# Kernel optimization log

Hardware: AMD Instinct MI355X
Metric: run time of the kernel (lower is better)

The kernel has to match this reference:

```python
import jax, jax.numpy as jnp
import numpy as np

B, T = 32, 4096
I_CND2 = 512      # 2 * size_i_cnd
EMB = 256         # size_i_embed_ar
H = 896           # size_h_rnn
FC = 896          # size_h_fc
O = 512           # size_o


def setup_inputs() -> dict:
    key = jax.random.key(0)
    ks = jax.random.split(key, 8)
    s = 0.02
    return {
        "reference_sample": jax.random.randint(ks[0], (B, T), 0, O),
        "i_cnd_series": jax.random.normal(ks[1], (B, T, I_CND2), dtype=jnp.float32),
        "emb": jax.random.normal(ks[2], (O, EMB), dtype=jnp.float32) * s,
        "w_ih": jax.random.normal(ks[3], (3 * H, EMB + I_CND2), dtype=jnp.float32) * s,
        "w_hh": jax.random.normal(ks[4], (3 * H, H), dtype=jnp.float32) * s,
        "b_ih": jnp.zeros((3 * H,), jnp.float32),
        "b_hh": jnp.zeros((3 * H,), jnp.float32),
        "fc1_w": jax.random.normal(ks[5], (FC, H), dtype=jnp.float32) * s,
        "fc1_b": jnp.zeros((FC,), jnp.float32),
        "fc2_w": jax.random.normal(ks[6], (O, FC), dtype=jnp.float32) * s,
        "fc2_b": jnp.zeros((O,), jnp.float32),
    }


def _gru_scan(gates_x, w_hh, b_hh):
    # gates_x: (B, T, 3H) precomputed input projections (torch gate order: r, z, n)
    h0 = jnp.zeros((gates_x.shape[0], H), gates_x.dtype)

    def step(h, gx):
        gh = h @ w_hh.T + b_hh
        xr, xz, xn = jnp.split(gx, 3, axis=-1)
        hr, hz, hn = jnp.split(gh, 3, axis=-1)
        r = jax.nn.sigmoid(xr + hr)
        z = jax.nn.sigmoid(xz + hz)
        n = jnp.tanh(xn + r * hn)
        h_new = (1.0 - z) * n + z * h
        return h_new, h_new

    _, hs = jax.lax.scan(step, h0, jnp.swapaxes(gates_x, 0, 1))  # (T, B, H)
    return jnp.swapaxes(hs, 0, 1)  # (B, T, H)


def reference(reference_sample, i_cnd_series, emb, w_ih, w_hh, b_ih, b_hh,
              fc1_w, fc1_b, fc2_w, fc2_b):
    # embedding + concat with conditioning
    x = jnp.concatenate([emb[reference_sample], i_cnd_series], axis=-1)  # (B,T,EMB+2C)
    # batch all input-side GRU matmuls (compute-dense), scan only hidden recurrence
    gates_x = jnp.einsum('btd,gd->btg', x, w_ih) + b_ih  # (B,T,3H)
    o_rnn = _gru_scan(gates_x, w_hh, b_hh)               # (B,T,H)
    hidden = jax.nn.relu(jnp.einsum('bth,fh->btf', o_rnn, fc1_w) + fc1_b)
    return jnp.einsum('btf,of->bto', hidden, fc2_w) + fc2_b  # (B,T,O)
```

## Files before the change

### kernel.cpp

```cpp
#include <hip/hip_runtime.h>

#define B_ 32
#define T_FULL 4096
#define EMB_ 256
#define XD_ 768
#define H_ 896
#define G3_ 2688
#define O_ 512
#define NWG_SCAN 28
#define UJ 32
#define THR_SCAN 768

typedef __attribute__((ext_vector_type(8))) short bf16x8;
typedef __attribute__((ext_vector_type(4))) float f32x4;

__device__ __forceinline__ f32x4 mfma16(bf16x8 a, bf16x8 b, f32x4 c) {
  return __builtin_amdgcn_mfma_f32_16x16x32_bf16(a, b, c, 0, 0, 0);
}

__device__ __forceinline__ unsigned short f2bf(float x) {
  union { float f; unsigned u; } v; v.f = x;
  unsigned r = v.u + 0x7fffu + ((v.u >> 16) & 1u);
  return (unsigned short)(r >> 16);
}
__device__ __forceinline__ float bf2f(unsigned short h) {
  union { float f; unsigned u; } v; v.u = ((unsigned)h) << 16;
  return v.f;
}

__device__ __forceinline__ unsigned long long aload64(const unsigned long long* p) {
  return __hip_atomic_load((unsigned long long*)p, __ATOMIC_RELAXED, __HIP_MEMORY_SCOPE_AGENT);
}
__device__ __forceinline__ unsigned aload32(const unsigned* p) {
  return __hip_atomic_load((unsigned*)p, __ATOMIC_RELAXED, __HIP_MEMORY_SCOPE_AGENT);
}
__device__ __forceinline__ void astore32(unsigned* p, unsigned v) {
  __hip_atomic_store(p, v, __ATOMIC_RELAXED, __HIP_MEMORY_SCOPE_AGENT);
}

__global__ __launch_bounds__(256) void cvt_bf16(const float* __restrict__ in,
                                                unsigned short* __restrict__ out, int n) {
  for (int i = blockIdx.x * 256 + threadIdx.x; i < n; i += gridDim.x * 256)
    out[i] = f2bf(in[i]);
}

template<int VAR>
__global__ __launch_bounds__(256) void gemm_bf16(
    const unsigned short* __restrict__ A,
    const int* __restrict__ sample,
    const float* __restrict__ icnd,
    const unsigned short* __restrict__ embb,
    const unsigned short* __restrict__ W,
    const float* __restrict__ bias,
    float* __restrict__ outf,
    unsigned short* __restrict__ outb,
    int t0) {
  constexpr int K = (VAR == 0) ? XD_ : H_;
  constexpr int N = (VAR == 0) ? G3_ : (VAR == 1 ? H_ : O_);
  constexpr int LDT = 48;
  __shared__ __align__(16) unsigned short Asl[128 * LDT];
  __shared__ __align__(16) unsigned short Bsl[128 * LDT];
  const int tid = threadIdx.x;
  const int rowBase = blockIdx.y * 128, colBase = blockIdx.x * 128;
  const int lane = tid & 63, wid = tid >> 6;
  const int wm = wid >> 1, wn = wid & 1;
  const int lr = lane & 15, lk = lane >> 4;
  const f32x4 fzero = {0.f, 0.f, 0.f, 0.f};
  f32x4 acc[4][4];
#pragma unroll
  for (int i = 0; i < 4; ++i)
#pragma unroll
    for (int j = 0; j < 4; ++j) acc[i][j] = fzero;

  for (int k0 = 0; k0 < K; k0 += 32) {
#pragma unroll
    for (int s = 0; s < 2; ++s) {
      const int seg = tid + s * 256;
      const int r = seg >> 2, kg = (seg & 3) * 8;
      const int kk = k0 + kg;
      bf16x8 va;
      if (VAR == 0) {
        const int rowG = rowBase + r;
        const int b = rowG & 31, t = t0 + (rowG >> 5);
        if (kk < EMB_) {
          const int e = sample[b * T_FULL + t];
          va = *(const bf16x8*)(embb + e * EMB_ + kk);
        } else {
          const float* p = icnd + ((size_t)(b * T_FULL + t)) * 512 + (kk - EMB_);
          const float4 f0 = *(const float4*)p;
          const float4 f1 = *(const float4*)(p + 4);
          va[0] = (short)f2bf(f0.x); va[1] = (short)f2bf(f0.y);
          va[2] = (short)f2bf(f0.z); va[3] = (short)f2bf(f0.w);
          va[4] = (short)f2bf(f1.x); va[5] = (short)f2bf(f1.y);
          va[6] = (short)f2bf(f1.z); va[7] = (short)f2bf(f1.w);
        }
      } else {
        va = *(const bf16x8*)(A + (size_t)(rowBase + r) * K + kk);
      }
      *(bf16x8*)(Asl + r * LDT + kg) = va;
      *(bf16x8*)(Bsl + r * LDT + kg) = *(const bf16x8*)(W + (size_t)(colBase + r) * K + kk);
    }
    __syncthreads();
    bf16x8 af[4], bfr[4];
#pragma unroll
    for (int mt = 0; mt < 4; ++mt)
      af[mt] = *(const bf16x8*)(Asl + (wm * 64 + mt * 16 + lr) * LDT + lk * 8);
#pragma unroll
    for (int nt = 0; nt < 4; ++nt)
      bfr[nt] = *(const bf16x8*)(Bsl + (wn * 64 + nt * 16 + lr) * LDT + lk * 8);
#pragma unroll
    for (int mt = 0; mt < 4; ++mt)
#pragma unroll
      for (int nt = 0; nt < 4; ++nt) acc[mt][nt] = mfma16(af[mt], bfr[nt], acc[mt][nt]);
    __syncthreads();
  }

#pragma unroll
  for (int mt = 0; mt < 4; ++mt) {
#pragma unroll
    for (int nt = 0; nt < 4; ++nt) {
      const int colG = colBase + wn * 64 + nt * 16 + lr;
      const float bv = bias[colG];
#pragma unroll
      for (int r = 0; r < 4; ++r) {
        const int rowG = rowBase + wm * 64 + mt * 16 + lk * 4 + r;
        const float v = acc[mt][nt][r] + bv;
        if (VAR == 0) {
          outf[(size_t)rowG * N + colG] = v;
        } else if (VAR == 1) {
          outb[(size_t)rowG * N + colG] = f2bf(fmaxf(v, 0.f));
        } else {
          const int b = rowG & 31, t = t0 + (rowG >> 5);
          outf[((size_t)(b * T_FULL + t)) * O_ + colG] = v;
        }
      }
    }
  }
}

__global__ __launch_bounds__(THR_SCAN) void scan_gru(
    const float* __restrict__ gates,
    const unsigned short* __restrict__ whh,
    const float* __restrict__ bhh,
    unsigned short* __restrict__ hhi,
    unsigned short* __restrict__ hlo,
    unsigned short* __restrict__ ornn,
    unsigned int* __restrict__ arr,
    int t0, int Tc) {
  __shared__ __align__(16) unsigned short hst[2][32 * H_];
  __shared__ float gh[3][32][UJ + 1];
  const int tid = threadIdx.x;
  const int j0 = blockIdx.x * UJ;
  const int lane = tid & 63, wid = tid >> 6;
  const int m = wid & 1;
  const int s = (wid >> 1) % 3;
  const int cn = wid / 6;
  const int lr = lane & 15, lk = lane >> 4;
  char* hbase = (char*)&hst[0][0];

  const int eb = tid >> 4, ec = (tid & 15) * 2;
  float hown0 = 0.f, hown1 = 0.f;
  float bh_r0 = 0.f, bh_r1 = 0.f, bh_z0 = 0.f, bh_z1 = 0.f, bh_n0 = 0.f, bh_n1 = 0.f;
  if (tid < 512) {
    const int j = j0 + ec;
    bh_r0 = bhh[j];          bh_r1 = bhh[j + 1];
    bh_z0 = bhh[H_ + j];     bh_z1 = bhh[H_ + j + 1];
    bh_n0 = bhh[2 * H_ + j]; bh_n1 = bhh[2 * H_ + j + 1];
    const int rb0 = (t0 + 1) & 1;
    const int o = rb0 * (32 * H_) + eb * H_ + j;
    const unsigned hi01 = aload32((const unsigned*)(hhi + o));
    const unsigned lo01 = aload32((const unsigned*)(hlo + o));
    hown0 = bf2f((unsigned short)(hi01 & 0xffff)) + bf2f((unsigned short)(lo01 & 0xffff));
    hown1 = bf2f((unsigned short)(hi01 >> 16)) + bf2f((unsigned short)(lo01 >> 16));
  }

  const unsigned short* wp = whh + (size_t)(s * H_ + j0 + cn * 16 + lr) * H_ + lk * 8;
  const int rrow = m * 16 + lr;
  const int rowb = rrow * 1792;
  const int sw_r = (rrow & 7) << 4;
  const f32x4 fzero = {0.f, 0.f, 0.f, 0.f};

  for (int tl = 0; tl < Tc; ++tl) {
    const int t = t0 + tl;
    const int rb = (t + 1) & 1, wb = t & 1;

    float2 pxr = {0.f, 0.f}, pxz = {0.f, 0.f}, pxn = {0.f, 0.f};
    if (tid < 512) {
      const float* gx = gates + ((size_t)tl * 32 + eb) * G3_;
      pxr = *(const float2*)(gx + j0 + ec);
      pxz = *(const float2*)(gx + H_ + j0 + ec);
      pxn = *(const float2*)(gx + 2 * H_ + j0 + ec);
    }

    {
      const unsigned long long* sh = (const unsigned long long*)(hhi + rb * (32 * H_));
      const unsigned long long* sl = (const unsigned long long*)(hlo + rb * (32 * H_));
#pragma unroll
      for (int k = 0; k < 10; ++k) {
        const int i = tid + k * THR_SCAN;
        if (i < 7168) {
          const unsigned long long vh = aload64(sh + i);
          const unsigned long long vl = aload64(sl + i);
          const int row = i / 224;
          const int cb = (i - row * 224) * 8;
          const int dst = row * 1792 + (cb ^ ((row & 7) << 4));
          *(unsigned long long*)(hbase + dst) = vh;
          *(unsigned long long*)(hbase + 57344 + dst) = vl;
        }
      }
    }
    __syncthreads();

    f32x4 a0 = fzero, a1 = fzero;
#pragma unroll
    for (int kk = 0; kk < 28; ++kk) {
      const int off = (lk * 16 + kk * 64) ^ sw_r;
      const bf16x8 ah = *(const bf16x8*)(hbase + rowb + off);
      const bf16x8 al = *(const bf16x8*)(hbase + 57344 + rowb + off);
      const bf16x8 bw = *(const bf16x8*)(wp + kk * 32);
      a0 = mfma16(ah, bw, a0);
      a1 = mfma16(al, bw, a1);
    }
#pragma unroll
    for (int r = 0; r < 4; ++r) gh[s][m * 16 + lk * 4 + r][cn * 16 + lr] = a0[r] + a1[r];
    __syncthreads();

    if (tid < 512) {
      const float ghr0 = gh[0][eb][ec] + bh_r0, ghr1 = gh[0][eb][ec + 1] + bh_r1;
      const float ghz0 = gh[1][eb][ec] + bh_z0, ghz1 = gh[1][eb][ec + 1] + bh_z1;
      const float ghn0 = gh[2][eb][ec] + bh_n0, ghn1 = gh[2][eb][ec + 1] + bh_n1;
      const float r0 = 1.f / (1.f + __expf(-(pxr.x + ghr0)));
      const float r1 = 1.f / (1.f + __expf(-(pxr.y + ghr1)));
      const float z0 = 1.f / (1.f + __expf(-(pxz.x + ghz0)));
      const float z1 = 1.f / (1.f + __expf(-(pxz.y + ghz1)));
      const float e0 = __expf(2.f * (pxn.x + r0 * ghn0));
      const float e1 = __expf(2.f * (pxn.y + r1 * ghn1));
      const float n0 = 1.f - 2.f / (e0 + 1.f);
      const float n1 = 1.f - 2.f / (e1 + 1.f);
      hown0 = (1.f - z0) * n0 + z0 * hown0;
      hown1 = (1.f - z1) * n1 + z1 * hown1;
      const unsigned short h0 = f2bf(hown0), h1 = f2bf(hown1);
      const unsigned short l0 = f2bf(hown0 - bf2f(h0)), l1 = f2bf(hown1 - bf2f(h1));
      const unsigned hi01 = (unsigned)h0 | ((unsigned)h1 << 16);
      const unsigned lo01 = (unsigned)l0 | ((unsigned)l1 << 16);
      const int o = wb * (32 * H_) + eb * H_ + j0 + ec;
      astore32((unsigned*)(hhi + o), hi01);
      astore32((unsigned*)(hlo + o), lo01);
      *(unsigned*)(ornn + ((size_t)tl * 32 + eb) * H_ + j0 + ec) = hi01;
    }

    asm volatile("s_waitcnt vmcnt(0)" ::: "memory");
    __syncthreads();
    if (wid == 0) {
      const unsigned tgt = (unsigned)(t + 1);
      if (lane == 0) astore32(arr + blockIdx.x, tgt);
      for (;;) {
        const unsigned v = (lane < NWG_SCAN) ? aload32(arr + lane) : tgt;
        if (__all(v >= tgt)) break;
        __builtin_amdgcn_s_sleep(1);
      }
    }
    __syncthreads();
  }
}

extern "C" void kernel_launch(void* const* d_in, const int* in_sizes, int n_in,
                              void* d_out, int out_size, void* d_ws, size_t ws_size,
                              hipStream_t stream) {
  (void)in_sizes; (void)n_in; (void)out_size;
  const int* sample = (const int*)d_in[0];
  const float* icnd = (const float*)d_in[1];
  const float* emb = (const float*)d_in[2];
  const float* wih = (const float*)d_in[3];
  const float* whh = (const float*)d_in[4];
  const float* bih = (const float*)d_in[5];
  const float* bhh = (const float*)d_in[6];
  const float* fc1w = (const float*)d_in[7];
  const float* fc1b = (const float*)d_in[8];
  const float* fc2w = (const float*)d_in[9];
  const float* fc2b = (const float*)d_in[10];
  float* out = (float*)d_out;
  char* ws = (char*)d_ws;

  size_t off = 0;
  auto alloc = [&](size_t bytes) {
    size_t o = off;
    off = (off + bytes + 255) & ~(size_t)255;
    return o;
  };
  const size_t o_arr = alloc(256);
  const size_t o_hhi = alloc((size_t)2 * 32 * H_ * 2);
  const size_t o_hlo = alloc((size_t)2 * 32 * H_ * 2);
  const size_t zero_end = off;
  const size_t o_emb = alloc((size_t)O_ * EMB_ * 2);
  const size_t o_wih = alloc((size_t)G3_ * XD_ * 2);
  const size_t o_whh = alloc((size_t)G3_ * H_ * 2);
  const size_t o_f1w = alloc((size_t)H_ * H_ * 2);
  const size_t o_f2w = alloc((size_t)O_ * H_ * 2);
  const size_t head = off;

  int Tc = 512;
  while (Tc > 8) {
    size_t need = head + (size_t)Tc * 32 * G3_ * 4 + 2 * ((size_t)Tc * 32 * H_ * 2) + 4096;
    if (need <= ws_size) break;
    Tc >>= 1;
  }
  const size_t o_gat = alloc((size_t)Tc * 32 * G3_ * 4);
  const size_t o_orn = alloc((size_t)Tc * 32 * H_ * 2);
  const size_t o_hid = alloc((size_t)Tc * 32 * H_ * 2);
  (void)o_gat; (void)o_orn; (void)o_hid;

  unsigned short* embb = (unsigned short*)(ws + o_emb);
  unsigned short* wihb = (unsigned short*)(ws + o_wih);
  unsigned short* whhb = (unsigned short*)(ws + o_whh);
  unsigned short* f1wb = (unsigned short*)(ws + o_f1w);
  unsigned short* f2wb = (unsigned short*)(ws + o_f2w);
  float* gat = (float*)(ws + o_gat);
  unsigned short* orn = (unsigned short*)(ws + o_orn);
  unsigned short* hid = (unsigned short*)(ws + o_hid);
  unsigned short* hhi = (unsigned short*)(ws + o_hhi);
  unsigned short* hlo = (unsigned short*)(ws + o_hlo);
  unsigned int* arr = (unsigned int*)(ws + o_arr);

  (void)hipMemsetAsync(ws, 0, zero_end, stream);

  cvt_bf16<<<512, 256, 0, stream>>>(emb, embb, O_ * EMB_);
  cvt_bf16<<<1024, 256, 0, stream>>>(wih, wihb, G3_ * XD_);
  cvt_bf16<<<1024, 256, 0, stream>>>(whh, whhb, G3_ * H_);
  cvt_bf16<<<512, 256, 0, stream>>>(fc1w, f1wb, H_ * H_);
  cvt_bf16<<<512, 256, 0, stream>>>(fc2w, f2wb, O_ * H_);

  const int nch = T_FULL / Tc;
  const int M = Tc * 32;
  for (int c = 0; c < nch; ++c) {
    const int t0 = c * Tc;
    gemm_bf16<0><<<dim3(G3_ / 128, M / 128), 256, 0, stream>>>(
        nullptr, sample, icnd, embb, wihb, bih, gat, nullptr, t0);
    scan_gru<<<NWG_SCAN, THR_SCAN, 0, stream>>>(gat, whhb, bhh, hhi, hlo, orn, arr, t0, Tc);
    gemm_bf16<1><<<dim3(H_ / 128, M / 128), 256, 0, stream>>>(
        orn, nullptr, nullptr, nullptr, f1wb, fc1b, nullptr, hid, t0);
    gemm_bf16<2><<<dim3(O_ / 128, M / 128), 256, 0, stream>>>(
        hid, nullptr, nullptr, nullptr, f2wb, fc2b, out, nullptr, t0);
  }
}
```

Before: 39.14 ms.

## Restructure GRU scan to 512 threads with fused hidden buffer and prefetch

```diff
diff --git a/kernel.cpp b/kernel.cpp
--- a/kernel.cpp
+++ b/kernel.cpp
@@ -8,8 +8,7 @@
 #define G3_ 2688
 #define O_ 512
 #define NWG_SCAN 28
-#define UJ 32
-#define THR_SCAN 768
+#define THR_SCAN 512
 
 typedef __attribute__((ext_vector_type(8))) short bf16x8;
 typedef __attribute__((ext_vector_type(4))) float f32x4;
@@ -142,93 +141,111 @@
     const float* __restrict__ gates,
     const unsigned short* __restrict__ whh,
     const float* __restrict__ bhh,
-    unsigned short* __restrict__ hhi,
-    unsigned short* __restrict__ hlo,
+    unsigned long long* __restrict__ hbuf,
     unsigned short* __restrict__ ornn,
     unsigned int* __restrict__ arr,
     int t0, int Tc) {
-  __shared__ __align__(16) unsigned short hst[2][32 * H_];
-  __shared__ float gh[3][32][UJ + 1];
+  __shared__ __align__(16) char hst[114688];
+  __shared__ float gh2[96][33];
   const int tid = threadIdx.x;
-  const int j0 = blockIdx.x * UJ;
+  const int j0 = blockIdx.x * 32;
   const int lane = tid & 63, wid = tid >> 6;
-  const int m = wid & 1;
-  const int s = (wid >> 1) % 3;
-  const int cn = wid / 6;
   const int lr = lane & 15, lk = lane >> 4;
-  char* hbase = (char*)&hst[0][0];
-
+  const int m = wid & 1, cw = wid >> 1;
   const int eb = tid >> 4, ec = (tid & 15) * 2;
-  float hown0 = 0.f, hown1 = 0.f;
-  float bh_r0 = 0.f, bh_r1 = 0.f, bh_z0 = 0.f, bh_z1 = 0.f, bh_n0 = 0.f, bh_n1 = 0.f;
-  if (tid < 512) {
+
+  float bh0, bh1, bh2, bh3, bh4, bh5;
+  float hown0, hown1;
+  {
     const int j = j0 + ec;
-    bh_r0 = bhh[j];          bh_r1 = bhh[j + 1];
-    bh_z0 = bhh[H_ + j];     bh_z1 = bhh[H_ + j + 1];
-    bh_n0 = bhh[2 * H_ + j]; bh_n1 = bhh[2 * H_ + j + 1];
+    bh0 = bhh[j];          bh1 = bhh[j + 1];
+    bh2 = bhh[H_ + j];     bh3 = bhh[H_ + j + 1];
+    bh4 = bhh[2 * H_ + j]; bh5 = bhh[2 * H_ + j + 1];
     const int rb0 = (t0 + 1) & 1;
-    const int o = rb0 * (32 * H_) + eb * H_ + j;
-    const unsigned hi01 = aload32((const unsigned*)(hhi + o));
-    const unsigned lo01 = aload32((const unsigned*)(hlo + o));
+    const unsigned short* hb = (const unsigned short*)hbuf;
+    const unsigned hi01 = aload32((const unsigned*)(hb + rb0 * 57344 + eb * 896 + j));
+    const unsigned lo01 = aload32((const unsigned*)(hb + rb0 * 57344 + 28672 + eb * 896 + j));
     hown0 = bf2f((unsigned short)(hi01 & 0xffff)) + bf2f((unsigned short)(lo01 & 0xffff));
     hown1 = bf2f((unsigned short)(hi01 >> 16)) + bf2f((unsigned short)(lo01 >> 16));
   }
 
-  const unsigned short* wp = whh + (size_t)(s * H_ + j0 + cn * 16 + lr) * H_ + lk * 8;
-  const int rrow = m * 16 + lr;
-  const int rowb = rrow * 1792;
-  const int sw_r = (rrow & 7) << 4;
+  const unsigned short* wp0;
+  const unsigned short* wp1;
+  const unsigned short* wp2;
+  {
+    const int cwc = (cw < 2) ? cw : 0;
+    const int t0i = cwc * 3;
+    wp0 = whh + (size_t)((t0i >> 1) * H_ + j0 + ((t0i & 1) << 4) + lr) * H_ + lk * 8;
+    const int t1i = cwc * 3 + 1;
+    wp1 = whh + (size_t)((t1i >> 1) * H_ + j0 + ((t1i & 1) << 4) + lr) * H_ + lk * 8;
+    const int t2i = cwc * 3 + 2;
+    wp2 = whh + (size_t)((t2i >> 1) * H_ + j0 + ((t2i & 1) << 4) + lr) * H_ + lk * 8;
+  }
+  const int rowb = (m * 16 + lr) * 1792;
+  const int sw = (lr & 7) << 4;
   const f32x4 fzero = {0.f, 0.f, 0.f, 0.f};
+
+  float2 pxr, pxz, pxn;
+  {
+    const float* gx = gates + (size_t)eb * G3_;
+    pxr = *(const float2*)(gx + j0 + ec);
+    pxz = *(const float2*)(gx + H_ + j0 + ec);
+    pxn = *(const float2*)(gx + 2 * H_ + j0 + ec);
+  }
 
   for (int tl = 0; tl < Tc; ++tl) {
     const int t = t0 + tl;
     const int rb = (t + 1) & 1, wb = t & 1;
 
-    float2 pxr = {0.f, 0.f}, pxz = {0.f, 0.f}, pxn = {0.f, 0.f};
-    if (tid < 512) {
-      const float* gx = gates + ((size_t)tl * 32 + eb) * G3_;
-      pxr = *(const float2*)(gx + j0 + ec);
-      pxz = *(const float2*)(gx + H_ + j0 + ec);
-      pxn = *(const float2*)(gx + 2 * H_ + j0 + ec);
-    }
-
     {
-      const unsigned long long* sh = (const unsigned long long*)(hhi + rb * (32 * H_));
-      const unsigned long long* sl = (const unsigned long long*)(hlo + rb * (32 * H_));
-#pragma unroll
-      for (int k = 0; k < 10; ++k) {
-        const int i = tid + k * THR_SCAN;
-        if (i < 7168) {
-          const unsigned long long vh = aload64(sh + i);
-          const unsigned long long vl = aload64(sl + i);
-          const int row = i / 224;
-          const int cb = (i - row * 224) * 8;
-          const int dst = row * 1792 + (cb ^ ((row & 7) << 4));
-          *(unsigned long long*)(hbase + dst) = vh;
-          *(unsigned long long*)(hbase + 57344 + dst) = vl;
-        }
-      }
-    }
-    __syncthreads();
-
-    f32x4 a0 = fzero, a1 = fzero;
-#pragma unroll
-    for (int kk = 0; kk < 28; ++kk) {
-      const int off = (lk * 16 + kk * 64) ^ sw_r;
-      const bf16x8 ah = *(const bf16x8*)(hbase + rowb + off);
-      const bf16x8 al = *(const bf16x8*)(hbase + 57344 + rowb + off);
-      const bf16x8 bw = *(const bf16x8*)(wp + kk * 32);
-      a0 = mfma16(ah, bw, a0);
-      a1 = mfma16(al, bw, a1);
-    }
-#pragma unroll
-    for (int r = 0; r < 4; ++r) gh[s][m * 16 + lk * 4 + r][cn * 16 + lr] = a0[r] + a1[r];
-    __syncthreads();
-
-    if (tid < 512) {
-      const float ghr0 = gh[0][eb][ec] + bh_r0, ghr1 = gh[0][eb][ec + 1] + bh_r1;
-      const float ghz0 = gh[1][eb][ec] + bh_z0, ghz1 = gh[1][eb][ec + 1] + bh_z1;
-      const float ghn0 = gh[2][eb][ec] + bh_n0, ghn1 = gh[2][eb][ec + 1] + bh_n1;
+      const unsigned long long* src = hbuf + (size_t)rb * 14336 + tid;
+      unsigned long long rg[28];
+#pragma unroll
+      for (int k = 0; k < 28; ++k) rg[k] = aload64(src + k * 512);
+#pragma unroll
+      for (int k = 0; k < 28; ++k) {
+        const int i = tid + k * 512;
+        const int p = (i >= 7168) ? 1 : 0;
+        const int w = i - p * 7168;
+        const int row = (int)(((unsigned)w * 18725u) >> 22);
+        const int cb = (w - row * 224) * 8;
+        const int dst = p * 57344 + row * 1792 + (cb ^ ((row & 7) << 4));
+        *(unsigned long long*)(hst + dst) = rg[k];
+      }
+    }
+    __syncthreads();
+
+    if (wid < 4) {
+      f32x4 acc[3][2];
+#pragma unroll
+      for (int u = 0; u < 3; ++u) { acc[u][0] = fzero; acc[u][1] = fzero; }
+#pragma unroll
+      for (int kk = 0; kk < 28; ++kk) {
+        const int off = (lk * 16 + kk * 64) ^ sw;
+        const bf16x8 ah = *(const bf16x8*)(hst + rowb + off);
+        const bf16x8 al = *(const bf16x8*)(hst + 57344 + rowb + off);
+        const bf16x8 b0 = *(const bf16x8*)(wp0 + kk * 32);
+        acc[0][0] = mfma16(ah, b0, acc[0][0]);
+        acc[0][1] = mfma16(al, b0, acc[0][1]);
+        const bf16x8 b1 = *(const bf16x8*)(wp1 + kk * 32);
+        acc[1][0] = mfma16(ah, b1, acc[1][0]);
+        acc[1][1] = mfma16(al, b1, acc[1][1]);
+        const bf16x8 b2 = *(const bf16x8*)(wp2 + kk * 32);
+        acc[2][0] = mfma16(ah, b2, acc[2][0]);
+        acc[2][1] = mfma16(al, b2, acc[2][1]);
+      }
+#pragma unroll
+      for (int u = 0; u < 3; ++u)
+#pragma unroll
+        for (int r = 0; r < 4; ++r)
+          gh2[(cw * 3 + u) * 16 + lr][m * 16 + lk * 4 + r] = acc[u][0][r] + acc[u][1][r];
+    }
+    __syncthreads();
+
+    {
+      const float ghr0 = gh2[ec][eb] + bh0,      ghr1 = gh2[ec + 1][eb] + bh1;
+      const float ghz0 = gh2[32 + ec][eb] + bh2, ghz1 = gh2[33 + ec][eb] + bh3;
+      const float ghn0 = gh2[64 + ec][eb] + bh4, ghn1 = gh2[65 + ec][eb] + bh5;
       const float r0 = 1.f / (1.f + __expf(-(pxr.x + ghr0)));
       const float r1 = 1.f / (1.f + __expf(-(pxr.y + ghr1)));
       const float z0 = 1.f / (1.f + __expf(-(pxz.x + ghz0)));
@@ -243,17 +260,24 @@
       const unsigned short l0 = f2bf(hown0 - bf2f(h0)), l1 = f2bf(hown1 - bf2f(h1));
       const unsigned hi01 = (unsigned)h0 | ((unsigned)h1 << 16);
       const unsigned lo01 = (unsigned)l0 | ((unsigned)l1 << 16);
-      const int o = wb * (32 * H_) + eb * H_ + j0 + ec;
-      astore32((unsigned*)(hhi + o), hi01);
-      astore32((unsigned*)(hlo + o), lo01);
-      *(unsigned*)(ornn + ((size_t)tl * 32 + eb) * H_ + j0 + ec) = hi01;
+      unsigned short* hb = (unsigned short*)hbuf;
+      const int o = wb * 57344 + eb * 896 + j0 + ec;
+      astore32((unsigned*)(hb + o), hi01);
+      astore32((unsigned*)(hb + o + 28672), lo01);
+      *(unsigned*)(ornn + ((size_t)tl * 32 + eb) * 896 + j0 + ec) = hi01;
     }
 
     asm volatile("s_waitcnt vmcnt(0)" ::: "memory");
     __syncthreads();
+    const unsigned tgt = (unsigned)(t + 1);
+    if (tid == 0) astore32(arr + blockIdx.x, tgt);
+    if (tl + 1 < Tc) {
+      const float* gx = gates + ((size_t)(tl + 1) * 32 + eb) * G3_;
+      pxr = *(const float2*)(gx + j0 + ec);
+      pxz = *(const float2*)(gx + H_ + j0 + ec);
+      pxn = *(const float2*)(gx + 2 * H_ + j0 + ec);
+    }
     if (wid == 0) {
-      const unsigned tgt = (unsigned)(t + 1);
-      if (lane == 0) astore32(arr + blockIdx.x, tgt);
       for (;;) {
         const unsigned v = (lane < NWG_SCAN) ? aload32(arr + lane) : tgt;
         if (__all(v >= tgt)) break;
@@ -289,8 +313,7 @@
     return o;
   };
   const size_t o_arr = alloc(256);
-  const size_t o_hhi = alloc((size_t)2 * 32 * H_ * 2);
-  const size_t o_hlo = alloc((size_t)2 * 32 * H_ * 2);
+  const size_t o_h = alloc((size_t)2 * 2 * 32 * H_ * 2);
   const size_t zero_end = off;
   const size_t o_emb = alloc((size_t)O_ * EMB_ * 2);
   const size_t o_wih = alloc((size_t)G3_ * XD_ * 2);
@@ -318,8 +341,7 @@
   float* gat = (float*)(ws + o_gat);
   unsigned short* orn = (unsigned short*)(ws + o_orn);
   unsigned short* hid = (unsigned short*)(ws + o_hid);
-  unsigned short* hhi = (unsigned short*)(ws + o_hhi);
-  unsigned short* hlo = (unsigned short*)(ws + o_hlo);
+  unsigned long long* hbuf = (unsigned long long*)(ws + o_h);
   unsigned int* arr = (unsigned int*)(ws + o_arr);
 
   (void)hipMemsetAsync(ws, 0, zero_end, stream);
@@ -336,7 +358,7 @@
     const int t0 = c * Tc;
     gemm_bf16<0><<<dim3(G3_ / 128, M / 128), 256, 0, stream>>>(
         nullptr, sample, icnd, embb, wihb, bih, gat, nullptr, t0);
-    scan_gru<<<NWG_SCAN, THR_SCAN, 0, stream>>>(gat, whhb, bhh, hhi, hlo, orn, arr, t0, Tc);
+    scan_gru<<<NWG_SCAN, THR_SCAN, 0, stream>>>(gat, whhb, bhh, hbuf, orn, arr, t0, Tc);
     gemm_bf16<1><<<dim3(H_ / 128, M / 128), 256, 0, stream>>>(
         orn, nullptr, nullptr, nullptr, f1wb, fc1b, nullptr, hid, t0);
     gemm_bf16<2><<<dim3(O_ / 128, M / 128), 256, 0, stream>>>(
```

New measurement: 55.31 ms. 41.3% more time.

## Keep W_hh in registers, use 32x32 MFMA, pre-swizzled global hidden state

Applied to the files above, without the earlier changes.

```diff
diff --git a/kernel.cpp b/kernel.cpp
--- a/kernel.cpp
+++ b/kernel.cpp
@@ -8,14 +8,17 @@
 #define G3_ 2688
 #define O_ 512
 #define NWG_SCAN 28
-#define UJ 32
 #define THR_SCAN 768
 
 typedef __attribute__((ext_vector_type(8))) short bf16x8;
 typedef __attribute__((ext_vector_type(4))) float f32x4;
+typedef __attribute__((ext_vector_type(16))) float f32x16;
 
 __device__ __forceinline__ f32x4 mfma16(bf16x8 a, bf16x8 b, f32x4 c) {
   return __builtin_amdgcn_mfma_f32_16x16x32_bf16(a, b, c, 0, 0, 0);
+}
+__device__ __forceinline__ f32x16 mfma32(bf16x8 a, bf16x8 b, f32x16 c) {
+  return __builtin_amdgcn_mfma_f32_32x32x16_bf16(a, b, c, 0, 0, 0);
 }
 
 __device__ __forceinline__ unsigned short f2bf(float x) {
@@ -36,6 +39,12 @@
 }
 __device__ __forceinline__ void astore32(unsigned* p, unsigned v) {
   __hip_atomic_store(p, v, __ATOMIC_RELAXED, __HIP_MEMORY_SCOPE_AGENT);
+}
+
+__device__ __forceinline__ int hswz(int row, int cb) {
+  const int g = cb >> 4;
+  const int gs = (g & ~15) | ((g & 15) ^ (row & 15));
+  return row * 1792 + (gs << 4) + (cb & 15);
 }
 
 __global__ __launch_bounds__(256) void cvt_bf16(const float* __restrict__ in,
@@ -142,48 +151,52 @@
     const float* __restrict__ gates,
     const unsigned short* __restrict__ whh,
     const float* __restrict__ bhh,
-    unsigned short* __restrict__ hhi,
-    unsigned short* __restrict__ hlo,
+    unsigned long long* __restrict__ hbuf,
     unsigned short* __restrict__ ornn,
     unsigned int* __restrict__ arr,
     int t0, int Tc) {
-  __shared__ __align__(16) unsigned short hst[2][32 * H_];
-  __shared__ float gh[3][32][UJ + 1];
+  __shared__ __align__(16) char hst[114688];
+  __shared__ float gh2f[2 * 96 * 32];
   const int tid = threadIdx.x;
-  const int j0 = blockIdx.x * UJ;
+  const int j0 = blockIdx.x * 32;
   const int lane = tid & 63, wid = tid >> 6;
-  const int m = wid & 1;
-  const int s = (wid >> 1) % 3;
-  const int cn = wid / 6;
-  const int lr = lane & 15, lk = lane >> 4;
-  char* hbase = (char*)&hst[0][0];
-
+  const int l31 = lane & 31, lhi = lane >> 5;
+  const int s = wid >> 2, kq = wid & 3;
+  const int ph = kq >> 1;
   const int eb = tid >> 4, ec = (tid & 15) * 2;
+
+  bf16x8 wreg[14];
+  {
+    const unsigned short* wrow = whh + (size_t)(s * H_ + j0 + l31) * H_ + kq * 224 + lhi * 8;
+#pragma unroll
+    for (int i = 0; i < 14; ++i) wreg[i] = *(const bf16x8*)(wrow + i * 16);
+  }
+
+  float bh0 = 0.f, bh1 = 0.f, bh2 = 0.f, bh3 = 0.f, bh4 = 0.f, bh5 = 0.f;
   float hown0 = 0.f, hown1 = 0.f;
-  float bh_r0 = 0.f, bh_r1 = 0.f, bh_z0 = 0.f, bh_z1 = 0.f, bh_n0 = 0.f, bh_n1 = 0.f;
   if (tid < 512) {
     const int j = j0 + ec;
-    bh_r0 = bhh[j];          bh_r1 = bhh[j + 1];
-    bh_z0 = bhh[H_ + j];     bh_z1 = bhh[H_ + j + 1];
-    bh_n0 = bhh[2 * H_ + j]; bh_n1 = bhh[2 * H_ + j + 1];
+    bh0 = bhh[j];          bh1 = bhh[j + 1];
+    bh2 = bhh[H_ + j];     bh3 = bhh[H_ + j + 1];
+    bh4 = bhh[2 * H_ + j]; bh5 = bhh[2 * H_ + j + 1];
     const int rb0 = (t0 + 1) & 1;
-    const int o = rb0 * (32 * H_) + eb * H_ + j;
-    const unsigned hi01 = aload32((const unsigned*)(hhi + o));
-    const unsigned lo01 = aload32((const unsigned*)(hlo + o));
+    const char* hb = (const char*)hbuf + rb0 * 114688;
+    const int off = hswz(eb, 2 * j);
+    const unsigned hi01 = aload32((const unsigned*)(hb + off));
+    const unsigned lo01 = aload32((const unsigned*)(hb + off + 57344));
     hown0 = bf2f((unsigned short)(hi01 & 0xffff)) + bf2f((unsigned short)(lo01 & 0xffff));
     hown1 = bf2f((unsigned short)(hi01 >> 16)) + bf2f((unsigned short)(lo01 >> 16));
   }
-
-  const unsigned short* wp = whh + (size_t)(s * H_ + j0 + cn * 16 + lr) * H_ + lk * 8;
-  const int rrow = m * 16 + lr;
-  const int rowb = rrow * 1792;
-  const int sw_r = (rrow & 7) << 4;
-  const f32x4 fzero = {0.f, 0.f, 0.f, 0.f};
 
   for (int tl = 0; tl < Tc; ++tl) {
     const int t = t0 + tl;
     const int rb = (t + 1) & 1, wb = t & 1;
 
+    {
+      const f32x4 z4 = {0.f, 0.f, 0.f, 0.f};
+      *(f32x4*)(gh2f + tid * 8) = z4;
+      *(f32x4*)(gh2f + tid * 8 + 4) = z4;
+    }
     float2 pxr = {0.f, 0.f}, pxz = {0.f, 0.f}, pxn = {0.f, 0.f};
     if (tid < 512) {
       const float* gx = gates + ((size_t)tl * 32 + eb) * G3_;
@@ -191,44 +204,61 @@
       pxz = *(const float2*)(gx + H_ + j0 + ec);
       pxn = *(const float2*)(gx + 2 * H_ + j0 + ec);
     }
-
     {
-      const unsigned long long* sh = (const unsigned long long*)(hhi + rb * (32 * H_));
-      const unsigned long long* sl = (const unsigned long long*)(hlo + rb * (32 * H_));
-#pragma unroll
-      for (int k = 0; k < 10; ++k) {
-        const int i = tid + k * THR_SCAN;
-        if (i < 7168) {
-          const unsigned long long vh = aload64(sh + i);
-          const unsigned long long vl = aload64(sl + i);
-          const int row = i / 224;
-          const int cb = (i - row * 224) * 8;
-          const int dst = row * 1792 + (cb ^ ((row & 7) << 4));
-          *(unsigned long long*)(hbase + dst) = vh;
-          *(unsigned long long*)(hbase + 57344 + dst) = vl;
-        }
-      }
-    }
-    __syncthreads();
-
-    f32x4 a0 = fzero, a1 = fzero;
-#pragma unroll
-    for (int kk = 0; kk < 28; ++kk) {
-      const int off = (lk * 16 + kk * 64) ^ sw_r;
-      const bf16x8 ah = *(const bf16x8*)(hbase + rowb + off);
-      const bf16x8 al = *(const bf16x8*)(hbase + 57344 + rowb + off);
-      const bf16x8 bw = *(const bf16x8*)(wp + kk * 32);
-      a0 = mfma16(ah, bw, a0);
-      a1 = mfma16(al, bw, a1);
-    }
-#pragma unroll
-    for (int r = 0; r < 4; ++r) gh[s][m * 16 + lk * 4 + r][cn * 16 + lr] = a0[r] + a1[r];
+      const unsigned long long* src = hbuf + (size_t)rb * 14336;
+      unsigned long long rg[10];
+#pragma unroll
+      for (int k = 0; k < 10; ++k) rg[k] = aload64(src + tid + k * 768);
+      __builtin_amdgcn_sched_barrier(0);
+#pragma unroll
+      for (int k = 0; k < 10; ++k)
+        *(unsigned long long*)(hst + (tid + k * 768) * 8) = rg[k];
+      unsigned long long rg2[9];
+#pragma unroll
+      for (int k = 0; k < 9; ++k) {
+        const int i = tid + (10 + k) * 768;
+        rg2[k] = (i < 14336) ? aload64(src + i) : 0ull;
+      }
+      __builtin_amdgcn_sched_barrier(0);
+#pragma unroll
+      for (int k = 0; k < 9; ++k) {
+        const int i = tid + (10 + k) * 768;
+        if (i < 14336) *(unsigned long long*)(hst + i * 8) = rg2[k];
+      }
+    }
+    __syncthreads();
+
+    {
+      f32x16 acc;
+#pragma unroll
+      for (int r = 0; r < 16; ++r) acc[r] = 0.f;
+#pragma unroll
+      for (int i = 0; i < 14; ++i) {
+        const int g = (kq * 14 + i) * 2 + lhi;
+        const int gs = (g & ~15) | ((g & 15) ^ (l31 & 15));
+        const int off = l31 * 1792 + (gs << 4);
+        const bf16x8 bh = *(const bf16x8*)(hst + off);
+        const bf16x8 bl = *(const bf16x8*)(hst + 57344 + off);
+        acc = mfma32(wreg[i], bh, acc);
+        acc = mfma32(wreg[i], bl, acc);
+      }
+#pragma unroll
+      for (int r = 0; r < 16; ++r) {
+        const int rowD = (r & 3) + 8 * (r >> 2) + 4 * lhi;
+        atomicAdd(&gh2f[(ph * 96 + s * 32 + rowD) * 32 + (l31 ^ rowD)], acc[r]);
+      }
+    }
     __syncthreads();
 
     if (tid < 512) {
-      const float ghr0 = gh[0][eb][ec] + bh_r0, ghr1 = gh[0][eb][ec + 1] + bh_r1;
-      const float ghz0 = gh[1][eb][ec] + bh_z0, ghz1 = gh[1][eb][ec + 1] + bh_z1;
-      const float ghn0 = gh[2][eb][ec] + bh_n0, ghn1 = gh[2][eb][ec + 1] + bh_n1;
+      const int b0 = (0 * 32 + ec) * 32, b1 = (1 * 32 + ec) * 32, b2 = (2 * 32 + ec) * 32;
+      const int c0 = eb ^ ec, c1 = eb ^ (ec + 1);
+      const float ghr0 = gh2f[b0 + c0] + gh2f[3072 + b0 + c0] + bh0;
+      const float ghr1 = gh2f[b0 + 32 + c1] + gh2f[3072 + b0 + 32 + c1] + bh1;
+      const float ghz0 = gh2f[b1 + c0] + gh2f[3072 + b1 + c0] + bh2;
+      const float ghz1 = gh2f[b1 + 32 + c1] + gh2f[3072 + b1 + 32 + c1] + bh3;
+      const float ghn0 = gh2f[b2 + c0] + gh2f[3072 + b2 + c0] + bh4;
+      const float ghn1 = gh2f[b2 + 32 + c1] + gh2f[3072 + b2 + 32 + c1] + bh5;
       const float r0 = 1.f / (1.f + __expf(-(pxr.x + ghr0)));
       const float r1 = 1.f / (1.f + __expf(-(pxr.y + ghr1)));
       const float z0 = 1.f / (1.f + __expf(-(pxz.x + ghz0)));
@@ -243,17 +273,18 @@
       const unsigned short l0 = f2bf(hown0 - bf2f(h0)), l1 = f2bf(hown1 - bf2f(h1));
       const unsigned hi01 = (unsigned)h0 | ((unsigned)h1 << 16);
       const unsigned lo01 = (unsigned)l0 | ((unsigned)l1 << 16);
-      const int o = wb * (32 * H_) + eb * H_ + j0 + ec;
-      astore32((unsigned*)(hhi + o), hi01);
-      astore32((unsigned*)(hlo + o), lo01);
+      char* hb = (char*)hbuf + wb * 114688;
+      const int off = hswz(eb, 2 * (j0 + ec));
+      astore32((unsigned*)(hb + off), hi01);
+      astore32((unsigned*)(hb + off + 57344), lo01);
       *(unsigned*)(ornn + ((size_t)tl * 32 + eb) * H_ + j0 + ec) = hi01;
     }
 
     asm volatile("s_waitcnt vmcnt(0)" ::: "memory");
     __syncthreads();
+    const unsigned tgt = (unsigned)(t + 1);
+    if (tid == 0) astore32(arr + blockIdx.x, tgt);
     if (wid == 0) {
-      const unsigned tgt = (unsigned)(t + 1);
-      if (lane == 0) astore32(arr + blockIdx.x, tgt);
       for (;;) {
         const unsigned v = (lane < NWG_SCAN) ? aload32(arr + lane) : tgt;
         if (__all(v >= tgt)) break;
@@ -289,8 +320,7 @@
     return o;
   };
   const size_t o_arr = alloc(256);
-  const size_t o_hhi = alloc((size_t)2 * 32 * H_ * 2);
-  const size_t o_hlo = alloc((size_t)2 * 32 * H_ * 2);
+  const size_t o_h = alloc((size_t)2 * 114688);
   const size_t zero_end = off;
   const size_t o_emb = alloc((size_t)O_ * EMB_ * 2);
   const size_t o_wih = alloc((size_t)G3_ * XD_ * 2);
@@ -318,8 +348,7 @@
   float* gat = (float*)(ws + o_gat);
   unsigned short* orn = (unsigned short*)(ws + o_orn);
   unsigned short* hid = (unsigned short*)(ws + o_hid);
-  unsigned short* hhi = (unsigned short*)(ws + o_hhi);
-  unsigned short* hlo = (unsigned short*)(ws + o_hlo);
+  unsigned long long* hbuf = (unsigned long long*)(ws + o_h);
   unsigned int* arr = (unsigned int*)(ws + o_arr);
 
   (void)hipMemsetAsync(ws, 0, zero_end, stream);
@@ -336,7 +365,7 @@
     const int t0 = c * Tc;
     gemm_bf16<0><<<dim3(G3_ / 128, M / 128), 256, 0, stream>>>(
         nullptr, sample, icnd, embb, wihb, bih, gat, nullptr, t0);
-    scan_gru<<<NWG_SCAN, THR_SCAN, 0, stream>>>(gat, whhb, bhh, hhi, hlo, orn, arr, t0, Tc);
+    scan_gru<<<NWG_SCAN, THR_SCAN, 0, stream>>>(gat, whhb, bhh, hbuf, orn, arr, t0, Tc);
     gemm_bf16<1><<<dim3(H_ / 128, M / 128), 256, 0, stream>>>(
         orn, nullptr, nullptr, nullptr, f1wb, fc1b, nullptr, hid, t0);
     gemm_bf16<2><<<dim3(O_ / 128, M / 128), 256, 0, stream>>>(
```

After: 88.20 ms. +125.3%, slower.
